# Kernel optimization log

Measured on AMD Instinct MI355X. Metric: run time of the kernel, lower is better.

## Reference

```python
import jax, jax.numpy as jnp
import numpy as np

N = 8192          # num atoms
K = 32            # neighbors per atom (init kwarg k)
CUTOFF = 10.0     # init kwarg cutoff
NUM_MOLS = 128


def setup_inputs() -> dict:
    key = jax.random.key(0)
    k1, k2 = jax.random.split(key)
    pos = jax.random.normal(k1, (N, 3), dtype=jnp.float32)
    batch = jnp.sort(jax.random.randint(k2, (N,), 0, NUM_MOLS)).astype(jnp.int32)
    return {"pos": pos, "batch": batch}


def _pairwise_dist(pos):
    # ||x_i - x_j|| via the gram-matrix expansion; avoids an [N,N,3] intermediate.
    sq_norm = jnp.sum(pos * pos, axis=-1)                     # [N]
    sq = sq_norm[:, None] + sq_norm[None, :] - 2.0 * (pos @ pos.T)  # [N,N]
    sq = jnp.maximum(sq, 0.0)
    # safe sqrt: exact 0 on the diagonal without nan-producing sqrt'(0) in grads
    safe = jnp.where(sq > 0, sq, 1.0)
    return jnp.where(sq > 0, jnp.sqrt(safe), 0.0)


def reference(pos, batch):
    n = pos.shape[0]
    pdist = _pairwise_dist(pos)                               # [N,N]
    rows = jnp.arange(n)
    diag = rows[:, None] == rows[None, :]
    cross = batch[:, None] != batch[None, :]
    outer = pdist > CUTOFF
    mask = diag | cross | outer
    pdist = jnp.where(mask, CUTOFF, pdist)
    neg_w, indices = jax.lax.top_k(-pdist, K)                 # [N,K] each
    rows_e = jnp.broadcast_to(rows[:, None], indices.shape)
    edge_index = jnp.stack([indices.reshape(-1), rows_e.reshape(-1)])  # [2, N*K]
    edge_weight = -neg_w.reshape(-1)                          # [N*K]
    return edge_index, edge_weight
```

## Files before the change

### kernel.cpp

```cpp
#include <hip/hip_runtime.h>


#define CUTOFF_F 10.0f
#define ROWS_PER_BLOCK 4

__device__ __forceinline__ float readlane_f(float v, int lane) {
    return __int_as_float(__builtin_amdgcn_readlane(__float_as_int(v), lane));
}
__device__ __forceinline__ int readlane_i(int v, int lane) {
    return __builtin_amdgcn_readlane(v, lane);
}

__device__ __forceinline__ float dist_v(float4 pr, float4 pc, bool diag) {
    if (diag) return CUTOFF_F;
    float dot = __fadd_rn(__fadd_rn(__fmul_rn(pr.x, pc.x), __fmul_rn(pr.y, pc.y)),
                          __fmul_rn(pr.z, pc.z));
    float sq = __fsub_rn(__fadd_rn(pr.w, pc.w), __fadd_rn(dot, dot));
    sq = fmaxf(sq, 0.0f);
    float d = (sq > 0.0f) ? __fsqrt_rn(sq) : 0.0f;
    return (d > CUTOFF_F) ? CUTOFF_F : d;
}

__device__ __forceinline__ float4 load_pos4(const float* __restrict__ pos, int g) {
    float x = pos[g * 3 + 0];
    float y = pos[g * 3 + 1];
    float z = pos[g * 3 + 2];
    float sq = __fadd_rn(__fadd_rn(__fmul_rn(x, x), __fmul_rn(y, y)), __fmul_rn(z, z));
    return make_float4(x, y, z, sq);
}

template <int NCH>
__device__ __forceinline__ void row_core_reg(const float* __restrict__ pos,
                                             float4 pr, int n, int lane,
                                             int start, int end, int r,
                                             float* __restrict__ out,
                                             int NK, int K) {
    float v[NCH];
    int   rk[NCH];
#pragma unroll
    for (int j = 0; j < NCH; ++j) {
        const int c = 64 * j + lane;
        v[j]  = (c < n) ? dist_v(pr, load_pos4(pos, start + c), (start + c) == r)
                        : CUTOFF_F;
        rk[j] = 0;
    }
#pragma unroll
    for (int jj = 0; jj < NCH; ++jj) {
        const int base = 64 * jj;
        const int lim  = (NCH == 1) ? n : min(n - base, 64);
#pragma unroll 4
        for (int cc = 0; cc < lim; ++cc) {
            const float vv = readlane_f(v[jj], cc);
            const int   g  = base + cc;
#pragma unroll
            for (int j = 0; j < NCH; ++j) {
                const int c = 64 * j + lane;
                rk[j] += (vv < v[j]) || (vv == v[j] && g < c);
            }
        }
    }
    int m = 0;
#pragma unroll
    for (int j = 0; j < NCH; ++j) {
        const int c = 64 * j + lane;
        m += __popcll(__ballot(c < n && v[j] < CUTOFF_F));
    }
#pragma unroll
    for (int j = 0; j < NCH; ++j) {
        const int c = 64 * j + lane;
        if (c < n && v[j] < CUTOFF_F && rk[j] < K) {
            const int o = r * K + rk[j];
            out[o]          = (float)(start + c);
            out[2 * NK + o] = v[j];
        }
    }
    for (int k2 = lane; k2 < K; k2 += 64)
        out[NK + r * K + k2] = (float)r;
    if (m < K) {
        const int mm = n - m;
        for (int fb = 0; fb < K - m; fb += 64) {
            const int t = fb + lane;
            const bool active = t < (K - m);
            int idx = 0;
            bool found = false;
            if (active) {
                if (t < start)            { idx = t;                      found = true; }
                else if (t - start >= mm) { idx = end + (t - start - mm); found = true; }
            }
            if (__any(active && !found)) {
                int cnt = 0;
#pragma unroll
                for (int jj = 0; jj < NCH; ++jj) {
                    const int base = 64 * jj;
                    const int lim  = min(n - base, 64);
                    for (int cc = 0; cc < lim; ++cc) {
                        if (readlane_f(v[jj], cc) == CUTOFF_F) {
                            if (active && !found && cnt == t - start) {
                                idx = start + base + cc; found = true;
                            }
                            ++cnt;
                        }
                    }
                }
            }
            if (active) {
                const int o = r * K + m + t;
                out[o]          = (float)idx;
                out[2 * NK + o] = CUTOFF_F;
            }
        }
    }
}

__device__ __attribute__((noinline))
int lower_bound_cold(const int* __restrict__ batch, int lo, int hi, int key) {
    while (lo < hi) {
        int mid = (lo + hi) >> 1;
        if (batch[mid] < key) lo = mid + 1; else hi = mid;
    }
    return lo;
}

__device__ __attribute__((noinline))
void row_core_fallback(const float* __restrict__ pos, float4 pr, int n, int lane,
                       int start, int end, int r, float* __restrict__ out,
                       int NK, int K) {
    int m = 0;
    for (int cb = 0; cb < n; cb += 64) {
        const int c = cb + lane;
        const float v = (c < n)
            ? dist_v(pr, load_pos4(pos, start + c), (start + c) == r) : CUTOFF_F;
        int rk = 0;
        for (int cc = 0; cc < n; ++cc) {
            const float vv = dist_v(pr, load_pos4(pos, start + cc), (start + cc) == r);
            rk += (vv < v) || (vv == v && cc < c);
        }
        if (c < n && v < CUTOFF_F && rk < K) {
            const int o = r * K + rk;
            out[o]          = (float)(start + c);
            out[2 * NK + o] = v;
        }
        m += __popcll(__ballot(c < n && v < CUTOFF_F));
    }
    for (int k2 = lane; k2 < K; k2 += 64)
        out[NK + r * K + k2] = (float)r;
    if (m < K) {
        const int mm = n - m;
        for (int fb = 0; fb < K - m; fb += 64) {
            const int t = fb + lane;
            const bool active = t < (K - m);
            int idx = 0; bool found = false;
            if (active) {
                if (t < start)            { idx = t;                      found = true; }
                else if (t - start >= mm) { idx = end + (t - start - mm); found = true; }
            }
            if (__any(active && !found)) {
                int cnt = 0;
                for (int cc = 0; cc < n; ++cc) {
                    if (dist_v(pr, load_pos4(pos, start + cc), (start + cc) == r)
                        == CUTOFF_F) {
                        if (active && !found && cnt == t - start) {
                            idx = start + cc; found = true;
                        }
                        ++cnt;
                    }
                }
            }
            if (active) {
                const int o = r * K + m + t;
                out[o]          = (float)idx;
                out[2 * NK + o] = CUTOFF_F;
            }
        }
    }
}

__global__ __launch_bounds__(256, 8)
void knn_fused_kernel(const float* __restrict__ pos,
                      const int* __restrict__ batch,
                      float* __restrict__ out,
                      int N, int K) {
    const int w    = threadIdx.x >> 6;
    const int lane = threadIdx.x & 63;
    const int r    = blockIdx.x * ROWS_PER_BLOCK + w;
    if (r >= N) return;
    const int NK = N * K;

    const int iu = r - 63 + lane;
    const int id = r + 1 + lane;
    const int au = batch[max(iu, 0)];
    const int ad = batch[min(id, N - 1)];
    const float4 pr = load_pos4(pos, r);

    const int b = readlane_i(au, 63);

    const unsigned long long mu = __ballot(iu >= 0 && au == b);
    int start;
    if (mu != ~0ull) {
        start = r - __builtin_clzll(~mu) + 1;
    } else {
        const int iu2 = r - 127 + lane;
        const unsigned long long mu2 =
            __ballot(iu2 >= 0 && batch[max(iu2, 0)] == b);
        if (mu2 != ~0ull)           start = r - 63 - __builtin_clzll(~mu2);
        else if (r - 127 <= 0)      start = 0;
        else                        start = lower_bound_cold(batch, 0, r, b);
    }

    const unsigned long long md = __ballot(id < N && ad == b);
    int end;
    if (md != ~0ull) {
        end = r + 1 + __builtin_ctzll(~md);
    } else {
        const int id2 = r + 65 + lane;
        const unsigned long long md2 =
            __ballot(id2 < N && batch[min(id2, N - 1)] == b);
        if (md2 != ~0ull)           end = r + 65 + __builtin_ctzll(~md2);
        else if (r + 129 >= N)      end = N;
        else                        end = lower_bound_cold(batch, r + 1, N, b + 1);
    }

    const int n = end - start;

    if      (n <= 64)  row_core_reg<1>(pos, pr, n, lane, start, end, r, out, NK, K);
    else if (n <= 128) row_core_reg<2>(pos, pr, n, lane, start, end, r, out, NK, K);
    else               row_core_fallback(pos, pr, n, lane, start, end, r, out, NK, K);
}

extern "C" void kernel_launch(void* const* d_in, const int* in_sizes, int n_in,
                              void* d_out, int out_size, void* d_ws, size_t ws_size,
                              hipStream_t stream) {
    const float* pos   = (const float*)d_in[0];
    const int*   batch = (const int*)d_in[1];
    float*       out   = (float*)d_out;

    const int N = in_sizes[1];
    const int K = out_size / (3 * N);

    const int grid = (N + ROWS_PER_BLOCK - 1) / ROWS_PER_BLOCK;
    knn_fused_kernel<<<grid, 256, 0, stream>>>(pos, batch, out, N, K);
}
```

Measured before the change: 66.55 us.

## Replace per-lane rank counting with wavefront bitonic sort of packed keys

Each row's per-lane distances are packed with their column index into 64-bit keys and sorted across the wavefront with a bitonic network built on xor shuffles. This replaces the O(n) readlane rank-counting loop with O(log^2 n) shuffle stages. Ties are broken by index through the key packing, and the fill path for masked entries is kept. Each 64-bit shuffle costs two 32-bit shuffles, so the stage count and the shuffle latency set the cost.

```diff
diff --git a/kernel.cpp b/kernel.cpp
--- a/kernel.cpp
+++ b/kernel.cpp
@@ -9,6 +9,11 @@
 }
 __device__ __forceinline__ int readlane_i(int v, int lane) {
     return __builtin_amdgcn_readlane(v, lane);
+}
+__device__ __forceinline__ unsigned long long shfl_xor_u64(unsigned long long x, int m) {
+    const int lo = __shfl_xor((int)(unsigned)(x & 0xffffffffull), m, 64);
+    const int hi = __shfl_xor((int)(unsigned)(x >> 32), m, 64);
+    return ((unsigned long long)(unsigned)hi << 32) | (unsigned)lo;
 }
 
 __device__ __forceinline__ float dist_v(float4 pr, float4 pc, bool diag) {
@@ -29,87 +34,146 @@
     return make_float4(x, y, z, sq);
 }
 
+__device__ __forceinline__ unsigned long long pack_key(float v, int c) {
+    return ((unsigned long long)(unsigned)__float_as_int(v) << 32) | (unsigned)c;
+}
+
+__device__ __forceinline__ unsigned long long bitonic64(unsigned long long key, int lane) {
+#pragma unroll
+    for (int k = 2; k <= 64; k <<= 1) {
+#pragma unroll
+        for (int j = k >> 1; j > 0; j >>= 1) {
+            const unsigned long long pk = shfl_xor_u64(key, j);
+            const bool take_min = (((lane & j) == 0) == ((lane & k) == 0));
+            key = ((pk < key) == take_min) ? pk : key;
+        }
+    }
+    return key;
+}
+
+__device__ __forceinline__ void bitonic128(unsigned long long& ka,
+                                           unsigned long long& kb, int lane) {
+#pragma unroll
+    for (int k = 2; k <= 128; k <<= 1) {
+#pragma unroll
+        for (int j = k >> 1; j > 0; j >>= 1) {
+            if (j == 64) {
+                const bool alt = ka < kb;
+                const unsigned long long mn = alt ? ka : kb;
+                const unsigned long long mx = alt ? kb : ka;
+                ka = mn; kb = mx;
+            } else {
+                const unsigned long long pa = shfl_xor_u64(ka, j);
+                const unsigned long long pb = shfl_xor_u64(kb, j);
+                const bool low = ((lane & j) == 0);
+                const bool upA = ((lane & k) == 0);
+                const bool upB = (k == 64) ? false : upA;
+                ka = ((pa < ka) == (low == upA)) ? pa : ka;
+                kb = ((pb < kb) == (low == upB)) ? pb : kb;
+            }
+        }
+    }
+}
+
 template <int NCH>
-__device__ __forceinline__ void row_core_reg(const float* __restrict__ pos,
-                                             float4 pr, int n, int lane,
-                                             int start, int end, int r,
-                                             float* __restrict__ out,
-                                             int NK, int K) {
-    float v[NCH];
-    int   rk[NCH];
-#pragma unroll
-    for (int j = 0; j < NCH; ++j) {
-        const int c = 64 * j + lane;
-        v[j]  = (c < n) ? dist_v(pr, load_pos4(pos, start + c), (start + c) == r)
-                        : CUTOFF_F;
-        rk[j] = 0;
-    }
-#pragma unroll
-    for (int jj = 0; jj < NCH; ++jj) {
-        const int base = 64 * jj;
-        const int lim  = (NCH == 1) ? n : min(n - base, 64);
-#pragma unroll 4
-        for (int cc = 0; cc < lim; ++cc) {
-            const float vv = readlane_f(v[jj], cc);
-            const int   g  = base + cc;
-#pragma unroll
-            for (int j = 0; j < NCH; ++j) {
-                const int c = 64 * j + lane;
-                rk[j] += (vv < v[j]) || (vv == v[j] && g < c);
-            }
-        }
-    }
-    int m = 0;
-#pragma unroll
-    for (int j = 0; j < NCH; ++j) {
-        const int c = 64 * j + lane;
-        m += __popcll(__ballot(c < n && v[j] < CUTOFF_F));
-    }
-#pragma unroll
-    for (int j = 0; j < NCH; ++j) {
-        const int c = 64 * j + lane;
-        if (c < n && v[j] < CUTOFF_F && rk[j] < K) {
-            const int o = r * K + rk[j];
-            out[o]          = (float)(start + c);
-            out[2 * NK + o] = v[j];
-        }
+__device__ __forceinline__ void do_fill(const float* v, int m, int K, int lane,
+                                        int start, int end, int n, int r, int NK,
+                                        float* __restrict__ out) {
+    const int mm = n - m;
+    for (int fb = 0; fb < K - m; fb += 64) {
+        const int t = fb + lane;
+        const bool active = t < (K - m);
+        int idx = 0;
+        bool found = false;
+        if (active) {
+            if (t < start)            { idx = t;                      found = true; }
+            else if (t - start >= mm) { idx = end + (t - start - mm); found = true; }
+        }
+        if (__any(active && !found)) {
+            int cnt = 0;
+#pragma unroll
+            for (int jj = 0; jj < NCH; ++jj) {
+                const int base = 64 * jj;
+                const int lim  = min(n - base, 64);
+                for (int cc = 0; cc < lim; ++cc) {
+                    if (readlane_f(v[jj], cc) == CUTOFF_F) {
+                        if (active && !found && cnt == t - start) {
+                            idx = start + base + cc; found = true;
+                        }
+                        ++cnt;
+                    }
+                }
+            }
+        }
+        if (active) {
+            const int o = r * K + m + t;
+            out[o]          = (float)idx;
+            out[2 * NK + o] = CUTOFF_F;
+        }
+    }
+}
+
+__device__ __forceinline__ void row_core_sort64(const float* __restrict__ pos,
+                                                float4 pr, int n, int lane,
+                                                int start, int end, int r,
+                                                float* __restrict__ out,
+                                                int NK, int K) {
+    const int c = lane;
+    float v[1];
+    v[0] = (c < n) ? dist_v(pr, load_pos4(pos, start + c), (start + c) == r)
+                   : CUTOFF_F;
+    unsigned long long key = pack_key(v[0], c);
+    key = bitonic64(key, lane);
+
+    const float vs = __int_as_float((int)(unsigned)(key >> 32));
+    const int   cs = (int)(unsigned)(key & 0xffffffffull);
+    if (lane < K && vs < CUTOFF_F) {
+        const int o = r * K + lane;
+        out[o]          = (float)(start + cs);
+        out[2 * NK + o] = vs;
     }
     for (int k2 = lane; k2 < K; k2 += 64)
         out[NK + r * K + k2] = (float)r;
-    if (m < K) {
-        const int mm = n - m;
-        for (int fb = 0; fb < K - m; fb += 64) {
-            const int t = fb + lane;
-            const bool active = t < (K - m);
-            int idx = 0;
-            bool found = false;
-            if (active) {
-                if (t < start)            { idx = t;                      found = true; }
-                else if (t - start >= mm) { idx = end + (t - start - mm); found = true; }
-            }
-            if (__any(active && !found)) {
-                int cnt = 0;
-#pragma unroll
-                for (int jj = 0; jj < NCH; ++jj) {
-                    const int base = 64 * jj;
-                    const int lim  = min(n - base, 64);
-                    for (int cc = 0; cc < lim; ++cc) {
-                        if (readlane_f(v[jj], cc) == CUTOFF_F) {
-                            if (active && !found && cnt == t - start) {
-                                idx = start + base + cc; found = true;
-                            }
-                            ++cnt;
-                        }
-                    }
-                }
-            }
-            if (active) {
-                const int o = r * K + m + t;
-                out[o]          = (float)idx;
-                out[2 * NK + o] = CUTOFF_F;
-            }
-        }
-    }
+    const int m = __popcll(__ballot(v[0] < CUTOFF_F));
+    if (m < K) do_fill<1>(v, m, K, lane, start, end, n, r, NK, out);
+}
+
+__device__ __forceinline__ void row_core_sort128(const float* __restrict__ pos,
+                                                 float4 pr, int n, int lane,
+                                                 int start, int end, int r,
+                                                 float* __restrict__ out,
+                                                 int NK, int K) {
+    const int cA = lane, cB = 64 + lane;
+    float v[2];
+    v[0] = (cA < n) ? dist_v(pr, load_pos4(pos, start + cA), (start + cA) == r)
+                    : CUTOFF_F;
+    v[1] = (cB < n) ? dist_v(pr, load_pos4(pos, start + cB), (start + cB) == r)
+                    : CUTOFF_F;
+    unsigned long long ka = pack_key(v[0], cA);
+    unsigned long long kb = pack_key(v[1], cB);
+    bitonic128(ka, kb, lane);
+
+    const float vsa = __int_as_float((int)(unsigned)(ka >> 32));
+    const int   csa = (int)(unsigned)(ka & 0xffffffffull);
+    if (lane < K && vsa < CUTOFF_F) {
+        const int o = r * K + lane;
+        out[o]          = (float)(start + csa);
+        out[2 * NK + o] = vsa;
+    }
+    if (64 + lane < K) {
+        const float vsb = __int_as_float((int)(unsigned)(kb >> 32));
+        const int   csb = (int)(unsigned)(kb & 0xffffffffull);
+        if (vsb < CUTOFF_F) {
+            const int o = r * K + 64 + lane;
+            out[o]          = (float)(start + csb);
+            out[2 * NK + o] = vsb;
+        }
+    }
+    for (int k2 = lane; k2 < K; k2 += 64)
+        out[NK + r * K + k2] = (float)r;
+    const int m = __popcll(__ballot(v[0] < CUTOFF_F))
+                + __popcll(__ballot(v[1] < CUTOFF_F));
+    if (m < K) do_fill<2>(v, m, K, lane, start, end, n, r, NK, out);
 }
 
 __device__ __attribute__((noinline))
@@ -222,8 +286,8 @@
 
     const int n = end - start;
 
-    if      (n <= 64)  row_core_reg<1>(pos, pr, n, lane, start, end, r, out, NK, K);
-    else if (n <= 128) row_core_reg<2>(pos, pr, n, lane, start, end, r, out, NK, K);
+    if      (n <= 64)  row_core_sort64 (pos, pr, n, lane, start, end, r, out, NK, K);
+    else if (n <= 128) row_core_sort128(pos, pr, n, lane, start, end, r, out, NK, K);
     else               row_core_fallback(pos, pr, n, lane, start, end, r, out, NK, K);
 }
 
```

Result: faster. 64.96 us (-2.4%).
